# Optimization experiments

Measured on AMD Instinct MI355X. Metric: run time of the kernel, lower is better.

## Reference

```python
import jax, jax.numpy as jnp
import numpy as np

B = 4          # graphs
N = 8192       # coarse nodes (2048/graph)
M = 65536      # fine (skip) nodes (16384/graph)
E = 131072     # edges (32768/graph)
T = 16         # global tokens per graph
F_IN = 16      # dim of x and x_skip (concat -> in_channels = 32)
HID, OUT = 32, 16
ED, GD, EMB, H = 3, 1024, 64, 4
K = 3


def _make_pe(t, d):
    # PositionalEncoding buffer (sin/cos), deterministic constant
    position = np.arange(t, dtype=np.float32)[:, None]
    div = np.exp(np.arange(0, d, 2, dtype=np.float32) * (-np.log(10000.0) / d))
    pe = np.zeros((t, d), dtype=np.float32)
    pe[:, 0::2] = np.sin(position * div)
    pe[:, 1::2] = np.cos(position * div)
    return jnp.asarray(pe)


def setup_inputs():
    key = jax.random.key(0)
    ks = jax.random.split(key, 30)
    n, m, e = N // B, M // B, E // B
    inp = {}
    inp['x'] = jax.random.normal(ks[0], (N, F_IN), jnp.float32)
    inp['pos'] = jax.random.normal(ks[1], (N, 3), jnp.float32)
    inp['batch'] = jnp.repeat(jnp.arange(B), n)
    inp['x_skip'] = jax.random.normal(ks[2], (M, F_IN), jnp.float32)
    inp['pos_skip'] = jax.random.normal(ks[3], (M, 3), jnp.float32)
    inp['batch_skip'] = jnp.repeat(jnp.arange(B), m)
    off = jnp.repeat(jnp.arange(B) * m, e)
    inp['edge_index'] = jax.random.randint(ks[4], (2, E), 0, m) + off[None, :]
    inp['global_token'] = jax.random.normal(ks[5], (B * T, GD), jnp.float32)
    def lin(k, o, i, s):
        return jax.random.normal(k, (o, i), jnp.float32) * s
    inp['Wq_w'] = lin(ks[6], EMB, ED, 0.3); inp['Wq_b'] = jnp.zeros((EMB,), jnp.float32)
    inp['Wk_w'] = lin(ks[7], EMB, GD, 0.03); inp['Wk_b'] = jnp.zeros((EMB,), jnp.float32)
    inp['Wv_w'] = lin(ks[8], EMB, GD, 0.03); inp['Wv_b'] = jnp.zeros((EMB,), jnp.float32)
    inp['in_proj_w'] = lin(ks[9], 3 * EMB, EMB, 0.125); inp['in_proj_b'] = jnp.zeros((3 * EMB,), jnp.float32)
    inp['out_w'] = lin(ks[10], EMB, EMB, 0.125); inp['out_b'] = jnp.zeros((EMB,), jnp.float32)
    dims = [(2 * F_IN, HID), (HID, HID), (HID, OUT)]
    for i, (ci, co) in enumerate(dims):
        inp[f'nn_w{i}'] = lin(ks[11 + 3 * i], ci * co, ED + EMB, 0.05)
        inp[f'nn_b{i}'] = jnp.zeros((ci * co,), jnp.float32)
        inp[f'root{i}'] = jax.random.normal(ks[12 + 3 * i], (ci, co), jnp.float32) * (1.0 / np.sqrt(ci))
        inp[f'bias{i}'] = jnp.zeros((co,), jnp.float32)
    return inp


def reference(x, pos, batch, x_skip, pos_skip, batch_skip, edge_index, global_token,
              Wq_w, Wq_b, Wk_w, Wk_b, Wv_w, Wv_b, in_proj_w, in_proj_b, out_w, out_b,
              nn_w0, nn_b0, root0, bias0, nn_w1, nn_b1, root1, bias1, nn_w2, nn_b2, root2, bias2):
    # ---- knn_interpolate (k=3, inverse squared-distance weighting) ----
    # graphs are equal-sized by construction so per-graph knn == batched knn
    pos_b = pos.reshape(B, -1, 3)
    posk_b = pos_skip.reshape(B, -1, 3)
    d2 = ((posk_b ** 2).sum(-1)[:, :, None] + (pos_b ** 2).sum(-1)[:, None, :]
          - 2.0 * jnp.einsum('bmc,bnc->bmn', posk_b, pos_b))  # [B,m,n]
    neg, idx = jax.lax.top_k(-d2, K)                           # [B,m,K]
    w = 1.0 / jnp.maximum(-neg, 1e-16)
    x_b = x.reshape(B, -1, x.shape[-1])
    feats = jnp.take_along_axis(x_b[:, None, :, :], idx[:, :, :, None], axis=2)  # [B,m,K,F]
    xf = ((w[..., None] * feats).sum(2) / w.sum(2)[..., None]).reshape(M, -1)

    src, dst = edge_index[0], edge_index[1]
    pseudo = pos_skip[dst] - pos_skip[src]                     # patch_size is None
    edge_pos = (0.5 * (pos_skip[dst] + pos_skip[src])).reshape(B, -1, 3)
    gt = global_token.reshape(B, -1, global_token.shape[-1])
    pe = _make_pe(gt.shape[1], EMB)
    Q = edge_pos @ Wq_w.T + Wq_b                               # [B,Eb,EMB]
    Kt = gt @ Wk_w.T + Wk_b + pe                               # dropout in eval = identity
    Vt = gt @ Wv_w.T + Wv_b + pe
    # ---- MultiheadAttention (batch_first) ----
    wq, wk, wv = jnp.split(in_proj_w, 3, axis=0)
    bq, bk, bv = jnp.split(in_proj_b, 3, axis=0)
    hd = EMB // H
    def heads(t, w_, b_):
        t = t @ w_.T + b_
        return t.reshape(t.shape[0], t.shape[1], H, hd).transpose(0, 2, 1, 3)
    q, k_, v = heads(Q, wq, bq), heads(Kt, wk, bk), heads(Vt, wv, bv)
    att = jax.nn.softmax(jnp.einsum('bhqd,bhkd->bhqk', q, k_) / np.sqrt(hd).astype(np.float32), axis=-1)
    o = jnp.einsum('bhqk,bhkd->bhqd', att, v).transpose(0, 2, 1, 3).reshape(B, -1, EMB)
    o = o @ out_w.T + out_b
    pseudo = jnp.concatenate([pseudo, o.reshape(-1, EMB)], axis=-1)  # [E, 3+64]

    # ---- NNConv stack (gather -> edge MLP -> per-edge matmul -> scatter mean) ----
    h = jnp.concatenate([xf, x_skip], axis=1)                  # [M, 32]
    ones = jnp.ones((E,), jnp.float32)
    cnt = jnp.maximum(jax.ops.segment_sum(ones, dst, num_segments=M), 1.0)[:, None]
    for nw, nb, rt, bs in ((nn_w0, nn_b0, root0, bias0),
                           (nn_w1, nn_b1, root1, bias1),
                           (nn_w2, nn_b2, root2, bias2)):
        ci, co = rt.shape
        we = jax.nn.relu(pseudo @ nw.T + nb).reshape(E, ci, co)  # MLP (BN at default eval stats ~ identity)
        msg = jnp.einsum('ei,eio->eo', h[src], we)               # [E, co]
        aggr = jax.ops.segment_sum(msg, dst, num_segments=M) / cnt
        h = jax.nn.relu(aggr + h @ rt + bs)                      # drop_act=False -> relu every layer
    return h, pos_skip, batch_skip
```

## Files before the change

### kernel.cpp

```cpp
#include <hip/hip_runtime.h>
#include <math.h>

#define NB    4
#define NN    8192
#define MM    65536
#define EE    131072
#define NPG   2048

typedef short short8 __attribute__((ext_vector_type(8)));
typedef float f32x4  __attribute__((ext_vector_type(4)));

static __device__ inline unsigned short f2b(float f) {
    unsigned u = __float_as_uint(f);
    u += 0x7fffu + ((u >> 16) & 1u);
    return (unsigned short)(u >> 16);
}
static __device__ inline unsigned f2b_pack(float a, float b) {
    unsigned x = __float_as_uint(a); x += 0x7fffu + ((x >> 16) & 1u);
    unsigned y = __float_as_uint(b); y += 0x7fffu + ((y >> 16) & 1u);
    return (x >> 16) | (y & 0xffff0000u);
}
static __device__ inline short8 bc8(uint4 v) {
    union { uint4 u; short8 s; } c; c.u = v; return c.s;
}

__global__ __launch_bounds__(256)
void k_knn(const float* __restrict__ pos, const float* __restrict__ pos_skip,
           const float* __restrict__ x, const float* __restrict__ x_skip,
           const int* __restrict__ batch_skip,
           float* __restrict__ h0, float* __restrict__ out_pos,
           float* __restrict__ out_batch)
{
    __shared__ float4 cp[NPG];
    __shared__ float  pk[4][64][3];
    __shared__ float  wFin[64][3];
    __shared__ int    iFin[64][3];

    int tid = threadIdx.x;
    int g = blockIdx.x >> 8;
    int cbase = g * NPG;
    for (int c = tid; c < NPG; c += 256) {
        float px = pos[(cbase + c) * 3 + 0];
        float py = pos[(cbase + c) * 3 + 1];
        float pz = pos[(cbase + c) * 3 + 2];
        cp[c] = make_float4(-2.f * px, -2.f * py, -2.f * pz, px * px + py * py + pz * pz);
    }
    __syncthreads();

    int node = tid & 63;
    int slice = tid >> 6;
    int fbase = blockIdx.x * 64;
    int f = fbase + node;
    float fx = pos_skip[f * 3 + 0], fy = pos_skip[f * 3 + 1], fz = pos_skip[f * 3 + 2];
    float fqe = fx * fx + fy * fy + fz * fz + 1e-5f;

    float k0 = 3.4028235e38f, k1 = 3.4028235e38f, k2 = 3.4028235e38f;
    const float4* cps = cp + slice * 512;
#pragma unroll 8
    for (int l = 0; l < 512; ++l) {
        float4 cc = cps[l];
        float d = fqe + cc.w;
        d = fmaf(cc.x, fx, d);
        d = fmaf(cc.y, fy, d);
        d = fmaf(cc.z, fz, d);
        float key = __uint_as_float((__float_as_uint(d) & 0xFFFFFE00u) | (unsigned)l);
        float t = fmaxf(k1, key);
        k2 = fminf(k2, t);
        k1 = __builtin_amdgcn_fmed3f(k0, k1, key);
        k0 = fminf(k0, key);
    }
    pk[slice][node][0] = k0; pk[slice][node][1] = k1; pk[slice][node][2] = k2;
    __syncthreads();

    if (tid < 64) {
        int n = tid;
        int fn = fbase + n;
        float gx = pos_skip[fn * 3 + 0], gy = pos_skip[fn * 3 + 1], gz = pos_skip[fn * 3 + 2];
        float gq = gx * gx + gy * gy + gz * gz;
        unsigned long long m0 = ~0ull, m1 = ~0ull, m2 = ~0ull;
#pragma unroll
        for (int s = 0; s < 4; ++s)
#pragma unroll
            for (int r = 0; r < 3; ++r) {
                unsigned key = __float_as_uint(pk[s][n][r]);
                int c = s * 512 + (int)(key & 511u);
                float4 cc = cp[c];
                float d = gq + cc.w;
                d = fmaf(cc.x, gx, d);
                d = fmaf(cc.y, gy, d);
                d = fmaf(cc.z, gz, d);
                d = fmaxf(d, 0.f);
                unsigned long long kk = ((unsigned long long)__float_as_uint(d) << 32) | (unsigned)c;
                unsigned long long t1 = m0 > kk ? m0 : kk; m0 = m0 < kk ? m0 : kk;
                unsigned long long t2 = m1 > t1 ? m1 : t1; m1 = m1 < t1 ? m1 : t1;
                m2 = m2 < t2 ? m2 : t2;
            }
        float d0 = __uint_as_float((unsigned)(m0 >> 32));
        float d1 = __uint_as_float((unsigned)(m1 >> 32));
        float d2 = __uint_as_float((unsigned)(m2 >> 32));
        float w0 = 1.f / fmaxf(d0, 1e-16f);
        float w1 = 1.f / fmaxf(d1, 1e-16f);
        float w2 = 1.f / fmaxf(d2, 1e-16f);
        float inv = 1.f / (w0 + w1 + w2);
        wFin[n][0] = w0 * inv; wFin[n][1] = w1 * inv; wFin[n][2] = w2 * inv;
        iFin[n][0] = cbase + (int)(m0 & 2047u);
        iFin[n][1] = cbase + (int)(m1 & 2047u);
        iFin[n][2] = cbase + (int)(m2 & 2047u);
        out_pos[fn * 3 + 0] = gx; out_pos[fn * 3 + 1] = gy; out_pos[fn * 3 + 2] = gz;
        out_batch[fn] = (float)batch_skip[fn];
    }
    __syncthreads();

    int n2 = tid >> 2, part = tid & 3;
    int f2 = fbase + n2;
    float4* h04 = (float4*)(h0 + (size_t)f2 * 32);
    if (part < 2) {
        const float4* x4 = (const float4*)x;
        float w0 = wFin[n2][0], w1 = wFin[n2][1], w2 = wFin[n2][2];
        int a0 = iFin[n2][0] * 4, a1 = iFin[n2][1] * 4, a2 = iFin[n2][2] * 4;
#pragma unroll
        for (int j = 0; j < 2; ++j) {
            int cj = part * 2 + j;
            float4 v0 = x4[a0 + cj], v1 = x4[a1 + cj], v2 = x4[a2 + cj];
            float4 r;
            r.x = w0 * v0.x + w1 * v1.x + w2 * v2.x;
            r.y = w0 * v0.y + w1 * v1.y + w2 * v2.y;
            r.z = w0 * v0.z + w1 * v1.z + w2 * v2.z;
            r.w = w0 * v0.w + w1 * v1.w + w2 * v2.w;
            h04[cj] = r;
        }
    } else {
        const float4* xs4 = (const float4*)x_skip;
#pragma unroll
        for (int j = 0; j < 2; ++j) {
            int cj = (part - 2) * 2 + j;
            h04[4 + cj] = xs4[f2 * 4 + cj];
        }
    }
}

__global__ __launch_bounds__(128)
void k_tokens1(const float* __restrict__ gt,
               const float* __restrict__ Wk_w, const float* __restrict__ Wk_b,
               const float* __restrict__ Wv_w, const float* __restrict__ Wv_b,
               float* __restrict__ KtVt)
{
    int b = blockIdx.x >> 4;
    int t = blockIdx.x & 15;
    int which = threadIdx.x >> 6;
    int d = threadIdx.x & 63;
    const float* W = which ? Wv_w : Wk_w;
    const float* bias = which ? Wv_b : Wk_b;
    const float4* row = (const float4*)(gt + (size_t)(b * 16 + t) * 1024);
    const float4* wr = (const float4*)(W + (size_t)d * 1024);
    float acc = 0.f;
    for (int c = 0; c < 256; ++c) {
        float4 a = row[c], w = wr[c];
        acc += a.x * w.x; acc += a.y * w.y; acc += a.z * w.z; acc += a.w * w.w;
    }
    int i2 = d >> 1;
    float dv = expf((float)(2 * i2) * (-0.14391156831212787f));
    float ang = (float)t * dv;
    float pe = (d & 1) ? cosf(ang) : sinf(ang);
    KtVt[((size_t)(b * 2 + which) * 16 + t) * 64 + d] = acc + bias[d] + pe;
}

__global__ __launch_bounds__(256)
void k_tokens2(const float* __restrict__ KtVt,
               const float* __restrict__ in_proj_w, const float* __restrict__ in_proj_b,
               const float* __restrict__ out_w,
               const float* __restrict__ Wq_w, const float* __restrict__ Wq_b,
               float* __restrict__ Mfold, uint4* __restrict__ v2fG)
{
    int b = blockIdx.x;
    int tid = threadIdx.x;
    __shared__ float KtL[1024], VtL[1024], vv[1024], kproj[1024];
    __shared__ float v2L[4096];
    __shared__ float qWs[192], qbs[64];
    for (int idx = tid; idx < 1024; idx += 256) {
        KtL[idx] = KtVt[(size_t)(b * 2 + 0) * 1024 + idx];
        VtL[idx] = KtVt[(size_t)(b * 2 + 1) * 1024 + idx];
    }
    __syncthreads();
    for (int idx = tid; idx < 2048; idx += 256) {
        int which = idx >> 10; int td = idx & 1023; int t = td >> 6; int j = td & 63;
        int r = (which ? 128 : 64) + j;
        const float* w = in_proj_w + (size_t)r * 64;
        const float* src = which ? VtL : KtL;
        float acc = in_proj_b[r];
#pragma unroll 8
        for (int dd = 0; dd < 64; ++dd) acc += src[t * 64 + dd] * w[dd];
        if (which) vv[t * 64 + j] = acc;
        else kproj[t * 64 + j] = acc;
    }
    for (int idx = tid; idx < 192; idx += 256) {
        int c = idx >> 6; int j = idx & 63;
        float acc = 0.f;
        for (int dd = 0; dd < 64; ++dd) acc += in_proj_w[(size_t)j * 64 + dd] * Wq_w[dd * 3 + c];
        qWs[c * 64 + j] = acc;
    }
    for (int j = tid; j < 64; j += 256) {
        float acc = in_proj_b[j];
        for (int dd = 0; dd < 64; ++dd) acc += in_proj_w[(size_t)j * 64 + dd] * Wq_b[dd];
        qbs[j] = acc;
    }
    __syncthreads();
    for (int idx = tid; idx < 4096; idx += 256) {
        int jo = idx & 63; int th2 = idx >> 6; int h = th2 & 3; int t = th2 >> 2;
        float acc = 0.f;
#pragma unroll
        for (int dd = 0; dd < 16; ++dd)
            acc += vv[t * 64 + h * 16 + dd] * out_w[(size_t)jo * 64 + h * 16 + dd];
        v2L[(t * 4 + h) * 64 + jo] = acc;
    }
    {
        int th = tid >> 2, c = tid & 3;
        int t = th >> 2, h = th & 3;
        float acc = 0.f;
#pragma unroll
        for (int dd = h * 16; dd < h * 16 + 16; ++dd) {
            float w = (c == 0) ? qWs[dd] : (c == 1) ? qWs[64 + dd]
                    : (c == 2) ? qWs[128 + dd] : qbs[dd];
            acc += w * kproj[t * 64 + dd];
        }
        Mfold[((size_t)b * 64 + th) * 4 + c] = 0.25f * acc;
    }
    __syncthreads();
    for (int it = tid; it < 512; it += 256) {
        int lane = it & 63, fi = it >> 6;
        int mi = fi >> 1, step = fi & 1;
        int outd = mi * 16 + (lane & 15);
        int th0 = step * 32 + (lane >> 4) * 8;
        uint4 v;
        v.x = f2b_pack(v2L[(th0 + 0) * 64 + outd], v2L[(th0 + 1) * 64 + outd]);
        v.y = f2b_pack(v2L[(th0 + 2) * 64 + outd], v2L[(th0 + 3) * 64 + outd]);
        v.z = f2b_pack(v2L[(th0 + 4) * 64 + outd], v2L[(th0 + 5) * 64 + outd]);
        v.w = f2b_pack(v2L[(th0 + 6) * 64 + outd], v2L[(th0 + 7) * 64 + outd]);
        v2fG[((size_t)b * 8 + fi) * 64 + lane] = v;
    }
}

__global__ __launch_bounds__(256)
void k_edge_attn(const float* __restrict__ ps, const int* __restrict__ ei,
                 const float* __restrict__ Mfold, const uint4* __restrict__ v2f,
                 const float* __restrict__ ob,
                 unsigned short* __restrict__ Pf, float* __restrict__ cnt)
{
    __shared__ unsigned attL[4 * 64 * 34];
    int tid = threadIdx.x;
    int wave = tid >> 6, lane = tid & 63, q = lane >> 4, c15 = lane & 15;
    int g = blockIdx.x >> 7;
    int e = blockIdx.x * 256 + tid;
    int s = ei[e], d = ei[EE + e];
    atomicAdd(&cnt[d], 1.f);
    float sx = ps[s * 3], sy = ps[s * 3 + 1], sz = ps[s * 3 + 2];
    float dx = ps[d * 3], dy = ps[d * 3 + 1], dz = ps[d * 3 + 2];
    float px = dx - sx, py = dy - sy, pz = dz - sz;
    float ex = 0.5f * (dx + sx), ey = 0.5f * (dy + sy), ez = 0.5f * (dz + sz);

    const float4* Mg = (const float4*)Mfold + (size_t)g * 64;
    float sc[64];
#pragma unroll
    for (int th = 0; th < 64; ++th) {
        float4 m = Mg[th];
        sc[th] = ex * m.x + ey * m.y + ez * m.z + m.w;
    }
#pragma unroll
    for (int h = 0; h < 4; ++h) {
        float mx = sc[h];
#pragma unroll
        for (int t = 1; t < 16; ++t) mx = fmaxf(mx, sc[t * 4 + h]);
        float ssum = 0.f;
#pragma unroll
        for (int t = 0; t < 16; ++t) {
            float eo = expf(sc[t * 4 + h] - mx);
            sc[t * 4 + h] = eo; ssum += eo;
        }
        float inv = 1.f / ssum;
#pragma unroll
        for (int t = 0; t < 16; ++t) sc[t * 4 + h] *= inv;
    }
    unsigned* slab = attL + wave * 64 * 34;
#pragma unroll
    for (int k = 0; k < 16; ++k) {
        uint2 v;
        v.x = f2b_pack(sc[4 * k + 0], sc[4 * k + 1]);
        v.y = f2b_pack(sc[4 * k + 2], sc[4 * k + 3]);
        *(uint2*)&slab[lane * 34 + 2 * k] = v;
    }
    __syncthreads();

    uint4 v2a[4][2];
#pragma unroll
    for (int mi = 0; mi < 4; ++mi)
#pragma unroll
        for (int st = 0; st < 2; ++st)
            v2a[mi][st] = v2f[((size_t)g * 8 + mi * 2 + st) * 64 + lane];

    f32x4 acc[4][4];
#pragma unroll
    for (int mi = 0; mi < 4; ++mi)
#pragma unroll
        for (int nt = 0; nt < 4; ++nt) acc[mi][nt] = (f32x4){0.f, 0.f, 0.f, 0.f};

#pragma unroll
    for (int nt = 0; nt < 4; ++nt) {
        const unsigned* rb = &slab[(nt * 16 + c15) * 34];
        uint4 b0 = *(const uint4*)&rb[q * 4];
        uint4 b1 = *(const uint4*)&rb[16 + q * 4];
#pragma unroll
        for (int mi = 0; mi < 4; ++mi) {
            acc[mi][nt] = __builtin_amdgcn_mfma_f32_16x16x32_bf16(bc8(v2a[mi][0]), bc8(b0), acc[mi][nt], 0, 0, 0);
            acc[mi][nt] = __builtin_amdgcn_mfma_f32_16x16x32_bf16(bc8(v2a[mi][1]), bc8(b1), acc[mi][nt], 0, 0, 0);
        }
    }
    __syncthreads();

    float4 obv[4];
#pragma unroll
    for (int mi = 0; mi < 4; ++mi) obv[mi] = *(const float4*)(ob + mi * 16 + q * 4);
#pragma unroll
    for (int mi = 0; mi < 4; ++mi)
#pragma unroll
        for (int nt = 0; nt < 4; ++nt) {
            f32x4 a = acc[mi][nt];
            uint2 v;
            v.x = f2b_pack(a[0] + obv[mi].x, a[1] + obv[mi].y);
            v.y = f2b_pack(a[2] + obv[mi].z, a[3] + obv[mi].w);
            *(uint2*)&slab[(nt * 16 + c15) * 34 + mi * 8 + q * 2] = v;
        }
    __syncthreads();

    uint4* Pf4 = (uint4*)Pf;
#pragma unroll
    for (int et = 0; et < 4; ++et) {
        int etg = blockIdx.x * 16 + wave * 4 + et;
#pragma unroll
        for (int st = 0; st < 2; ++st) {
            uint4 w = *(const uint4*)&slab[(et * 16 + c15) * 34 + st * 16 + q * 4];
            Pf4[((size_t)etg * 3 + st) * 64 + lane] = w;
        }
    }
    int et2 = e >> 4, eL = e & 15;
    size_t tb = ((size_t)(et2 * 3 + 2) * 64 + 0 * 16 + eL) * 8;
    uint2 t0; t0.x = f2b_pack(px, py); t0.y = f2b_pack(pz, 1.0f);
    *(uint2*)(Pf + tb) = t0;
    uint2 z2; z2.x = 0u; z2.y = 0u;
    *(uint2*)(Pf + tb + 4) = z2;
#pragma unroll
    for (int quad = 1; quad < 4; ++quad) {
        size_t zb = ((size_t)(et2 * 3 + 2) * 64 + quad * 16 + eL) * 8;
        uint4 z4; z4.x = 0u; z4.y = 0u; z4.z = 0u; z4.w = 0u;
        *(uint4*)(Pf + zb) = z4;
    }
}

static __device__ inline void repack_one(const float* __restrict__ nw,
                                         const float* __restrict__ nb,
                                         unsigned short* __restrict__ Wf, int idx)
{
    int jj = idx & 7;
    int lane = (idx >> 3) & 63;
    int rest = idx >> 9;
    int s = rest % 3;
    int jt = rest / 3;
    int j = jt * 16 + (lane & 15);
    int k = s * 32 + (lane >> 4) * 8 + jj;
    float v;
    if (k < 64)       v = nw[(size_t)j * 67 + 3 + k];
    else if (k < 67)  v = nw[(size_t)j * 67 + (k - 64)];
    else if (k == 67) v = nb[j];
    else              v = 0.f;
    Wf[idx] = f2b(v);
}

__global__ __launch_bounds__(256)
void k_repackAll(const float* __restrict__ nw0, const float* __restrict__ nb0,
                 const float* __restrict__ nw1, const float* __restrict__ nb1,
                 const float* __restrict__ nw2, const float* __restrict__ nb2,
                 unsigned short* __restrict__ Wf0, unsigned short* __restrict__ Wf1,
                 unsigned short* __restrict__ Wf2)
{
    int idx = blockIdx.x * 256 + threadIdx.x;
    if (idx < 98304)        repack_one(nw0, nb0, Wf0, idx);
    else if (idx < 196608)  repack_one(nw1, nb1, Wf1, idx - 98304);
    else                    repack_one(nw2, nb2, Wf2, idx - 196608);
}

template<int CO>
__global__ __launch_bounds__(256, 4)
void k_conv_mfma(const uint4* __restrict__ Pf, const float* __restrict__ hin,
                 const int* __restrict__ ei, const uint4* __restrict__ Wf,
                 float* __restrict__ aggr)
{
    __shared__ float hL[128 * 36];
    __shared__ int sL[128];
    __shared__ int dL[128];
    constexpr int REDSZ = (CO == 16) ? 2 * 64 * 17 : 4;
    __shared__ float red[REDSZ];

    int tid = threadIdx.x;
    int e0 = blockIdx.x * 128;
    if (tid < 128) sL[tid] = ei[e0 + tid];
    else           dL[tid - 128] = ei[EE + e0 + (tid - 128)];
    __syncthreads();
    for (int idx = tid; idx < 1024; idx += 256) {
        int row = idx >> 3, c = idx & 7;
        const float4* hr = (const float4*)(hin + (size_t)sL[row] * 32);
        *(float4*)&hL[row * 36 + c * 4] = hr[c];
    }
    __syncthreads();

    int wave = tid >> 6, lane = tid & 63, quad = lane >> 4, col = lane & 15;
    int group = wave >> 1, half = wave & 1;

    uint4 a[4][3];
    int et0 = blockIdx.x * 8 + group * 4;
#pragma unroll
    for (int st = 0; st < 4; ++st)
#pragma unroll
        for (int s = 0; s < 3; ++s)
            a[st][s] = Pf[((size_t)(et0 + st) * 3 + s) * 64 + lane];

    float msg[4][4];
#pragma unroll
    for (int st = 0; st < 4; ++st)
#pragma unroll
        for (int r = 0; r < 4; ++r) msg[st][r] = 0.f;

    int ibase = (CO == 32) ? 0 : half * 16;
    constexpr int NI2 = (CO == 32) ? 16 : 8;

    for (int i2 = 0; i2 < NI2; ++i2) {
        float2 hv2[4][4];
#pragma unroll
        for (int st = 0; st < 4; ++st)
#pragma unroll
            for (int r = 0; r < 4; ++r)
                hv2[st][r] = *(const float2*)&hL[(group * 64 + st * 16 + quad * 4 + r) * 36
                                                 + ibase + i2 * 2];
#pragma unroll
        for (int ii = 0; ii < 2; ++ii) {
            int i = ibase + i2 * 2 + ii;
            int jt = (CO == 32) ? (i * 2 + half) : i;
            uint4 b0 = Wf[((size_t)jt * 3 + 0) * 64 + lane];
            uint4 b1 = Wf[((size_t)jt * 3 + 1) * 64 + lane];
            uint4 b2 = Wf[((size_t)jt * 3 + 2) * 64 + lane];
#pragma unroll
            for (int st = 0; st < 4; ++st) {
                f32x4 c = {0.f, 0.f, 0.f, 0.f};
                c = __builtin_amdgcn_mfma_f32_16x16x32_bf16(bc8(a[st][0]), bc8(b0), c, 0, 0, 0);
                c = __builtin_amdgcn_mfma_f32_16x16x32_bf16(bc8(a[st][1]), bc8(b1), c, 0, 0, 0);
                c = __builtin_amdgcn_mfma_f32_16x16x32_bf16(bc8(a[st][2]), bc8(b2), c, 0, 0, 0);
#pragma unroll
                for (int r = 0; r < 4; ++r) {
                    float hv = ii ? hv2[st][r].y : hv2[st][r].x;
                    msg[st][r] += hv * fmaxf(c[r], 0.f);
                }
            }
        }
    }

    if (CO == 32) {
#pragma unroll
        for (int st = 0; st < 4; ++st)
#pragma unroll
            for (int r = 0; r < 4; ++r) {
                int dv = dL[group * 64 + st * 16 + quad * 4 + r];
                atomicAdd(&aggr[(size_t)dv * 32 + half * 16 + col], msg[st][r]);
            }
    } else {
        if (half == 1) {
#pragma unroll
            for (int st = 0; st < 4; ++st)
#pragma unroll
                for (int r = 0; r < 4; ++r)
                    red[group * 64 * 17 + lane * 17 + st * 4 + r] = msg[st][r];
        }
        __syncthreads();
        if (half == 0) {
#pragma unroll
            for (int st = 0; st < 4; ++st)
#pragma unroll
                for (int r = 0; r < 4; ++r) {
                    float m = msg[st][r] + red[group * 64 * 17 + lane * 17 + st * 4 + r];
                    int dv = dL[group * 64 + st * 16 + quad * 4 + r];
                    atomicAdd(&aggr[(size_t)dv * 16 + col], m);
                }
        }
    }
}

template<int CO>
__global__ __launch_bounds__(256)
void k_update(float* __restrict__ aggr, const float* __restrict__ cnt,
              const float* __restrict__ hin, const float* __restrict__ root,
              const float* __restrict__ bias, float* __restrict__ hout)
{
    __shared__ float rL[32 * CO];
    __shared__ float bL[CO];
    int tid = threadIdx.x;
    for (int idx = tid; idx < 32 * CO; idx += 256) rL[idx] = root[idx];
    if (tid < CO) bL[tid] = bias[tid];
    __syncthreads();
    int gid = blockIdx.x * 256 + tid;
    int v = gid / CO;
    int o = gid % CO;
    float acc = aggr[gid] / fmaxf(cnt[v], 1.f) + bL[o];
    aggr[gid] = 0.f;
    const float* hr = hin + (size_t)v * 32;
#pragma unroll
    for (int i = 0; i < 32; ++i) acc += hr[i] * rL[i * CO + o];
    hout[gid] = fmaxf(acc, 0.f);
}

extern "C" void kernel_launch(void* const* d_in, const int* in_sizes, int n_in,
                              void* d_out, int out_size, void* d_ws, size_t ws_size,
                              hipStream_t stream)
{
    const float* x          = (const float*)d_in[0];
    const float* pos        = (const float*)d_in[1];
    const float* x_skip     = (const float*)d_in[3];
    const float* pos_skip   = (const float*)d_in[4];
    const int*   batch_skip = (const int*)  d_in[5];
    const int*   ei         = (const int*)  d_in[6];
    const float* gt         = (const float*)d_in[7];
    const float* Wq_w       = (const float*)d_in[8];
    const float* Wq_b       = (const float*)d_in[9];
    const float* Wk_w       = (const float*)d_in[10];
    const float* Wk_b       = (const float*)d_in[11];
    const float* Wv_w       = (const float*)d_in[12];
    const float* Wv_b       = (const float*)d_in[13];
    const float* in_proj_w  = (const float*)d_in[14];
    const float* in_proj_b  = (const float*)d_in[15];
    const float* out_w      = (const float*)d_in[16];
    const float* out_b      = (const float*)d_in[17];
    const float* nn_w0 = (const float*)d_in[18]; const float* nn_b0 = (const float*)d_in[19];
    const float* root0 = (const float*)d_in[20]; const float* bias0 = (const float*)d_in[21];
    const float* nn_w1 = (const float*)d_in[22]; const float* nn_b1 = (const float*)d_in[23];
    const float* root1 = (const float*)d_in[24]; const float* bias1 = (const float*)d_in[25];
    const float* nn_w2 = (const float*)d_in[26]; const float* nn_b2 = (const float*)d_in[27];
    const float* root2 = (const float*)d_in[28]; const float* bias2 = (const float*)d_in[29];

    char* wsb = (char*)d_ws;
    size_t off = 0;
    auto carve = [&](size_t bytes) { char* p = wsb + off; off += (bytes + 255) & ~(size_t)255; return p; };
    float* aggr = (float*)carve((size_t)MM * 32 * 4);
    float* cnt  = (float*)carve((size_t)MM * 4);
    float* hA   = (float*)carve((size_t)MM * 32 * 4);
    float* hB   = (float*)carve((size_t)MM * 32 * 4);
    unsigned short* Pf  = (unsigned short*)carve((size_t)EE * 96 * 2);
    unsigned short* Wf0 = (unsigned short*)carve((size_t)1024 * 96 * 2);
    unsigned short* Wf1 = (unsigned short*)carve((size_t)1024 * 96 * 2);
    unsigned short* Wf2 = (unsigned short*)carve((size_t)512 * 96 * 2);
    float* Mfold = (float*)carve((size_t)NB * 64 * 4 * 4);
    uint4* v2f   = (uint4*)carve((size_t)NB * 8 * 64 * 16);
    float* KtVt  = (float*)carve((size_t)NB * 2 * 16 * 64 * 4);

    float* h_final   = (float*)d_out;
    float* out_pos   = (float*)d_out + (size_t)MM * 16;
    float* out_batch = (float*)d_out + (size_t)MM * 19;

    hipMemsetAsync(aggr, 0, ((size_t)MM * 32 + MM) * sizeof(float), stream);

    k_tokens1<<<64, 128, 0, stream>>>(gt, Wk_w, Wk_b, Wv_w, Wv_b, KtVt);
    k_tokens2<<<NB, 256, 0, stream>>>(KtVt, in_proj_w, in_proj_b, out_w, Wq_w, Wq_b,
                                      Mfold, v2f);
    k_knn<<<MM / 64, 256, 0, stream>>>(pos, pos_skip, x, x_skip, batch_skip,
                                       hA, out_pos, out_batch);
    k_edge_attn<<<EE / 256, 256, 0, stream>>>(pos_skip, ei, Mfold, v2f, out_b,
                                              Pf, cnt);
    k_repackAll<<<960, 256, 0, stream>>>(nn_w0, nn_b0, nn_w1, nn_b1, nn_w2, nn_b2,
                                         Wf0, Wf1, Wf2);

    k_conv_mfma<32><<<EE / 128, 256, 0, stream>>>((const uint4*)Pf, hA, ei, (const uint4*)Wf0, aggr);
    k_update<32><<<(MM * 32) / 256, 256, 0, stream>>>(aggr, cnt, hA, root0, bias0, hB);
    k_conv_mfma<32><<<EE / 128, 256, 0, stream>>>((const uint4*)Pf, hB, ei, (const uint4*)Wf1, aggr);
    k_update<32><<<(MM * 32) / 256, 256, 0, stream>>>(aggr, cnt, hB, root1, bias1, hA);
    k_conv_mfma<16><<<EE / 128, 256, 0, stream>>>((const uint4*)Pf, hA, ei, (const uint4*)Wf2, aggr);
    k_update<16><<<(MM * 16) / 256, 256, 0, stream>>>(aggr, cnt, hA, root2, bias2, h_final);
}
```

Measured before the change: 365.4 us.

## Halve kNN block tile, stage coarse points in two LDS halves, refine from global

The kNN kernel now handles 32 fine nodes per block instead of 64, with 8 slices each scanning 128 candidates per pass. The coarse points of a graph are staged into LDS in two 1024-point halves, which halves the LDS footprint and should raise occupancy. Exact refinement now reloads candidate positions from global memory, and the dropped epsilon plus a wider index field in the key slightly change the approximate first-pass ranking. In exchange, each block loads the coarse-point array twice over, there are twice as many blocks, and there is an extra barrier per block.

New measurement: 366.2 us. About the same (+0.2%).

```diff
diff --git a/kernel.cpp b/kernel.cpp
--- a/kernel.cpp
+++ b/kernel.cpp
@@ -31,64 +31,72 @@
            float* __restrict__ h0, float* __restrict__ out_pos,
            float* __restrict__ out_batch)
 {
-    __shared__ float4 cp[NPG];
-    __shared__ float  pk[4][64][3];
-    __shared__ float  wFin[64][3];
-    __shared__ int    iFin[64][3];
+    __shared__ float4 cp[1024];
+    __shared__ float  pk[8][32][3];
+    __shared__ float  wFin[32][3];
+    __shared__ int    iFin[32][3];
 
     int tid = threadIdx.x;
-    int g = blockIdx.x >> 8;
+    int g = blockIdx.x >> 9;
     int cbase = g * NPG;
-    for (int c = tid; c < NPG; c += 256) {
-        float px = pos[(cbase + c) * 3 + 0];
-        float py = pos[(cbase + c) * 3 + 1];
-        float pz = pos[(cbase + c) * 3 + 2];
-        cp[c] = make_float4(-2.f * px, -2.f * py, -2.f * pz, px * px + py * py + pz * pz);
-    }
-    __syncthreads();
-
-    int node = tid & 63;
-    int slice = tid >> 6;
-    int fbase = blockIdx.x * 64;
+    int node = tid & 31;
+    int slice = tid >> 5;
+    int fbase = blockIdx.x * 32;
     int f = fbase + node;
     float fx = pos_skip[f * 3 + 0], fy = pos_skip[f * 3 + 1], fz = pos_skip[f * 3 + 2];
-    float fqe = fx * fx + fy * fy + fz * fz + 1e-5f;
 
     float k0 = 3.4028235e38f, k1 = 3.4028235e38f, k2 = 3.4028235e38f;
-    const float4* cps = cp + slice * 512;
+#pragma unroll
+    for (int p = 0; p < 2; ++p) {
+        if (p) __syncthreads();
+        for (int c = tid; c < 1024; c += 256) {
+            int cc = cbase + p * 1024 + c;
+            float px = pos[cc * 3 + 0];
+            float py = pos[cc * 3 + 1];
+            float pz = pos[cc * 3 + 2];
+            cp[c] = make_float4(-2.f * px, -2.f * py, -2.f * pz,
+                                px * px + py * py + pz * pz);
+        }
+        __syncthreads();
+        const float4* cps = cp + slice * 128;
+        unsigned ibase = (unsigned)(p * 128);
 #pragma unroll 8
-    for (int l = 0; l < 512; ++l) {
-        float4 cc = cps[l];
-        float d = fqe + cc.w;
-        d = fmaf(cc.x, fx, d);
-        d = fmaf(cc.y, fy, d);
-        d = fmaf(cc.z, fz, d);
-        float key = __uint_as_float((__float_as_uint(d) & 0xFFFFFE00u) | (unsigned)l);
-        float t = fmaxf(k1, key);
-        k2 = fminf(k2, t);
-        k1 = __builtin_amdgcn_fmed3f(k0, k1, key);
-        k0 = fminf(k0, key);
+        for (int l = 0; l < 128; ++l) {
+            float4 cc = cps[l];
+            float d = fmaf(cc.x, fx, cc.w);
+            d = fmaf(cc.y, fy, d);
+            d = fmaf(cc.z, fz, d);
+            float key = __uint_as_float((__float_as_uint(d) & 0xFFFFFF00u)
+                                        | (ibase + (unsigned)l));
+            float t = fmaxf(k1, key);
+            k2 = fminf(k2, t);
+            k1 = __builtin_amdgcn_fmed3f(k0, k1, key);
+            k0 = fminf(k0, key);
+        }
     }
     pk[slice][node][0] = k0; pk[slice][node][1] = k1; pk[slice][node][2] = k2;
     __syncthreads();
 
-    if (tid < 64) {
+    if (tid < 32) {
         int n = tid;
         int fn = fbase + n;
         float gx = pos_skip[fn * 3 + 0], gy = pos_skip[fn * 3 + 1], gz = pos_skip[fn * 3 + 2];
         float gq = gx * gx + gy * gy + gz * gz;
         unsigned long long m0 = ~0ull, m1 = ~0ull, m2 = ~0ull;
 #pragma unroll
-        for (int s = 0; s < 4; ++s)
+        for (int s = 0; s < 8; ++s)
 #pragma unroll
             for (int r = 0; r < 3; ++r) {
                 unsigned key = __float_as_uint(pk[s][n][r]);
-                int c = s * 512 + (int)(key & 511u);
-                float4 cc = cp[c];
-                float d = gq + cc.w;
-                d = fmaf(cc.x, gx, d);
-                d = fmaf(cc.y, gy, d);
-                d = fmaf(cc.z, gz, d);
+                unsigned pj = key & 255u;
+                int c = cbase + (int)((pj >> 7) * 1024u + (unsigned)s * 128u + (pj & 127u));
+                float px = pos[c * 3 + 0];
+                float py = pos[c * 3 + 1];
+                float pz = pos[c * 3 + 2];
+                float d = gq + (px * px + py * py + pz * pz);
+                d = fmaf(-2.f * px, gx, d);
+                d = fmaf(-2.f * py, gy, d);
+                d = fmaf(-2.f * pz, gz, d);
                 d = fmaxf(d, 0.f);
                 unsigned long long kk = ((unsigned long long)__float_as_uint(d) << 32) | (unsigned)c;
                 unsigned long long t1 = m0 > kk ? m0 : kk; m0 = m0 < kk ? m0 : kk;
@@ -103,39 +111,31 @@
         float w2 = 1.f / fmaxf(d2, 1e-16f);
         float inv = 1.f / (w0 + w1 + w2);
         wFin[n][0] = w0 * inv; wFin[n][1] = w1 * inv; wFin[n][2] = w2 * inv;
-        iFin[n][0] = cbase + (int)(m0 & 2047u);
-        iFin[n][1] = cbase + (int)(m1 & 2047u);
-        iFin[n][2] = cbase + (int)(m2 & 2047u);
+        iFin[n][0] = (int)(m0 & 0xffffffffull);
+        iFin[n][1] = (int)(m1 & 0xffffffffull);
+        iFin[n][2] = (int)(m2 & 0xffffffffull);
         out_pos[fn * 3 + 0] = gx; out_pos[fn * 3 + 1] = gy; out_pos[fn * 3 + 2] = gz;
         out_batch[fn] = (float)batch_skip[fn];
     }
     __syncthreads();
 
-    int n2 = tid >> 2, part = tid & 3;
+    int n2 = tid >> 3, part = tid & 7;
     int f2 = fbase + n2;
     float4* h04 = (float4*)(h0 + (size_t)f2 * 32);
-    if (part < 2) {
+    if (part < 4) {
         const float4* x4 = (const float4*)x;
         float w0 = wFin[n2][0], w1 = wFin[n2][1], w2 = wFin[n2][2];
         int a0 = iFin[n2][0] * 4, a1 = iFin[n2][1] * 4, a2 = iFin[n2][2] * 4;
-#pragma unroll
-        for (int j = 0; j < 2; ++j) {
-            int cj = part * 2 + j;
-            float4 v0 = x4[a0 + cj], v1 = x4[a1 + cj], v2 = x4[a2 + cj];
-            float4 r;
-            r.x = w0 * v0.x + w1 * v1.x + w2 * v2.x;
-            r.y = w0 * v0.y + w1 * v1.y + w2 * v2.y;
-            r.z = w0 * v0.z + w1 * v1.z + w2 * v2.z;
-            r.w = w0 * v0.w + w1 * v1.w + w2 * v2.w;
-            h04[cj] = r;
-        }
+        float4 v0 = x4[a0 + part], v1 = x4[a1 + part], v2 = x4[a2 + part];
+        float4 r;
+        r.x = w0 * v0.x + w1 * v1.x + w2 * v2.x;
+        r.y = w0 * v0.y + w1 * v1.y + w2 * v2.y;
+        r.z = w0 * v0.z + w1 * v1.z + w2 * v2.z;
+        r.w = w0 * v0.w + w1 * v1.w + w2 * v2.w;
+        h04[part] = r;
     } else {
         const float4* xs4 = (const float4*)x_skip;
-#pragma unroll
-        for (int j = 0; j < 2; ++j) {
-            int cj = (part - 2) * 2 + j;
-            h04[4 + cj] = xs4[f2 * 4 + cj];
-        }
+        h04[part] = xs4[f2 * 4 + (part - 4)];
     }
 }
 
@@ -566,7 +566,7 @@
     k_tokens1<<<64, 128, 0, stream>>>(gt, Wk_w, Wk_b, Wv_w, Wv_b, KtVt);
     k_tokens2<<<NB, 256, 0, stream>>>(KtVt, in_proj_w, in_proj_b, out_w, Wq_w, Wq_b,
                                       Mfold, v2f);
-    k_knn<<<MM / 64, 256, 0, stream>>>(pos, pos_skip, x, x_skip, batch_skip,
+    k_knn<<<MM / 32, 256, 0, stream>>>(pos, pos_skip, x, x_skip, batch_skip,
                                        hA, out_pos, out_batch);
     k_edge_attn<<<EE / 256, 256, 0, stream>>>(pos_skip, ei, Mfold, v2f, out_b,
                                               Pf, cnt);
```

## Precompute coarse-point table once and stream it via uniform loads in kNN

Applied to the files above, without the earlier changes.

The per-block LDS staging of the 2048 coarse positions (with the -2p and |p|^2 transform) moves into k_tokens1, which writes a global float4 table once. The kNN inner loop now reads that table at a wave-uniform address (readfirstlane slice), so the loads can become scalar or broadcast loads, and the query-norm add is dropped from the ranking distance. This removes the LDS fill and its barrier from each of the 1024 blocks. In exchange, the inner loop depends on global or cache latency instead of LDS, and the refinement step recomputes exact distances from pos.

After: 369.9 us. Within noise of the previous version (+1.2%).

```diff
diff --git a/kernel.cpp b/kernel.cpp
--- a/kernel.cpp
+++ b/kernel.cpp
@@ -25,13 +25,13 @@
 }
 
 __global__ __launch_bounds__(256)
-void k_knn(const float* __restrict__ pos, const float* __restrict__ pos_skip,
+void k_knn(const float4* __restrict__ cpre, const float* __restrict__ pos,
+           const float* __restrict__ pos_skip,
            const float* __restrict__ x, const float* __restrict__ x_skip,
            const int* __restrict__ batch_skip,
            float* __restrict__ h0, float* __restrict__ out_pos,
            float* __restrict__ out_batch)
 {
-    __shared__ float4 cp[NPG];
     __shared__ float  pk[4][64][3];
     __shared__ float  wFin[64][3];
     __shared__ int    iFin[64][3];
@@ -39,28 +39,20 @@
     int tid = threadIdx.x;
     int g = blockIdx.x >> 8;
     int cbase = g * NPG;
-    for (int c = tid; c < NPG; c += 256) {
-        float px = pos[(cbase + c) * 3 + 0];
-        float py = pos[(cbase + c) * 3 + 1];
-        float pz = pos[(cbase + c) * 3 + 2];
-        cp[c] = make_float4(-2.f * px, -2.f * py, -2.f * pz, px * px + py * py + pz * pz);
-    }
-    __syncthreads();
-
     int node = tid & 63;
     int slice = tid >> 6;
     int fbase = blockIdx.x * 64;
     int f = fbase + node;
     float fx = pos_skip[f * 3 + 0], fy = pos_skip[f * 3 + 1], fz = pos_skip[f * 3 + 2];
-    float fqe = fx * fx + fy * fy + fz * fz + 1e-5f;
+
+    int slice_u = __builtin_amdgcn_readfirstlane(slice);
+    const float4* cw = cpre + (size_t)cbase + (size_t)slice_u * 512;
 
     float k0 = 3.4028235e38f, k1 = 3.4028235e38f, k2 = 3.4028235e38f;
-    const float4* cps = cp + slice * 512;
 #pragma unroll 8
     for (int l = 0; l < 512; ++l) {
-        float4 cc = cps[l];
-        float d = fqe + cc.w;
-        d = fmaf(cc.x, fx, d);
+        float4 cc = cw[l];
+        float d = fmaf(cc.x, fx, cc.w);
         d = fmaf(cc.y, fy, d);
         d = fmaf(cc.z, fz, d);
         float key = __uint_as_float((__float_as_uint(d) & 0xFFFFFE00u) | (unsigned)l);
@@ -83,12 +75,14 @@
 #pragma unroll
             for (int r = 0; r < 3; ++r) {
                 unsigned key = __float_as_uint(pk[s][n][r]);
-                int c = s * 512 + (int)(key & 511u);
-                float4 cc = cp[c];
-                float d = gq + cc.w;
-                d = fmaf(cc.x, gx, d);
-                d = fmaf(cc.y, gy, d);
-                d = fmaf(cc.z, gz, d);
+                int c = cbase + s * 512 + (int)(key & 511u);
+                float px = pos[c * 3 + 0];
+                float py = pos[c * 3 + 1];
+                float pz = pos[c * 3 + 2];
+                float d = gq + (px * px + py * py + pz * pz);
+                d = fmaf(-2.f * px, gx, d);
+                d = fmaf(-2.f * py, gy, d);
+                d = fmaf(-2.f * pz, gz, d);
                 d = fmaxf(d, 0.f);
                 unsigned long long kk = ((unsigned long long)__float_as_uint(d) << 32) | (unsigned)c;
                 unsigned long long t1 = m0 > kk ? m0 : kk; m0 = m0 < kk ? m0 : kk;
@@ -103,9 +97,9 @@
         float w2 = 1.f / fmaxf(d2, 1e-16f);
         float inv = 1.f / (w0 + w1 + w2);
         wFin[n][0] = w0 * inv; wFin[n][1] = w1 * inv; wFin[n][2] = w2 * inv;
-        iFin[n][0] = cbase + (int)(m0 & 2047u);
-        iFin[n][1] = cbase + (int)(m1 & 2047u);
-        iFin[n][2] = cbase + (int)(m2 & 2047u);
+        iFin[n][0] = (int)(m0 & 0xffffffffull);
+        iFin[n][1] = (int)(m1 & 0xffffffffull);
+        iFin[n][2] = (int)(m2 & 0xffffffffull);
         out_pos[fn * 3 + 0] = gx; out_pos[fn * 3 + 1] = gy; out_pos[fn * 3 + 2] = gz;
         out_batch[fn] = (float)batch_skip[fn];
     }
@@ -143,8 +137,17 @@
 void k_tokens1(const float* __restrict__ gt,
                const float* __restrict__ Wk_w, const float* __restrict__ Wk_b,
                const float* __restrict__ Wv_w, const float* __restrict__ Wv_b,
+               const float* __restrict__ pos, float4* __restrict__ cpre,
                float* __restrict__ KtVt)
 {
+    int cgid = blockIdx.x * 128 + threadIdx.x;
+    {
+        float px = pos[cgid * 3 + 0];
+        float py = pos[cgid * 3 + 1];
+        float pz = pos[cgid * 3 + 2];
+        cpre[cgid] = make_float4(-2.f * px, -2.f * py, -2.f * pz,
+                                 px * px + py * py + pz * pz);
+    }
     int b = blockIdx.x >> 4;
     int t = blockIdx.x & 15;
     int which = threadIdx.x >> 6;
@@ -556,6 +559,7 @@
     float* Mfold = (float*)carve((size_t)NB * 64 * 4 * 4);
     uint4* v2f   = (uint4*)carve((size_t)NB * 8 * 64 * 16);
     float* KtVt  = (float*)carve((size_t)NB * 2 * 16 * 64 * 4);
+    float4* cpre = (float4*)carve((size_t)NN * 16);
 
     float* h_final   = (float*)d_out;
     float* out_pos   = (float*)d_out + (size_t)MM * 16;
@@ -563,10 +567,10 @@
 
     hipMemsetAsync(aggr, 0, ((size_t)MM * 32 + MM) * sizeof(float), stream);
 
-    k_tokens1<<<64, 128, 0, stream>>>(gt, Wk_w, Wk_b, Wv_w, Wv_b, KtVt);
+    k_tokens1<<<64, 128, 0, stream>>>(gt, Wk_w, Wk_b, Wv_w, Wv_b, pos, cpre, KtVt);
     k_tokens2<<<NB, 256, 0, stream>>>(KtVt, in_proj_w, in_proj_b, out_w, Wq_w, Wq_b,
                                       Mfold, v2f);
-    k_knn<<<MM / 64, 256, 0, stream>>>(pos, pos_skip, x, x_skip, batch_skip,
+    k_knn<<<MM / 64, 256, 0, stream>>>(cpre, pos, pos_skip, x, x_skip, batch_skip,
                                        hA, out_pos, out_batch);
     k_edge_attn<<<EE / 256, 256, 0, stream>>>(pos_skip, ei, Mfold, v2f, out_b,
                                               Pf, cnt);
```
